# Performance work log

Hardware: AMD Instinct MI355X
Metric: run time of the kernel (lower is better)

Reference implementation:

```python
import jax, jax.numpy as jnp
import numpy as np

B, D = 8192, 128
REGULARIZE = 0.01


def setup_inputs() -> dict:
    key = jax.random.key(0)
    ks = jax.random.split(key, 8)
    s = 1.0 / np.sqrt(D)
    X = jax.random.normal(ks[0], (B, D), dtype=jnp.float32)
    y = jax.random.randint(ks[1], (B,), 0, 100, dtype=jnp.int64 if jax.config.read('jax_enable_x64') else jnp.int32)
    W1 = jax.random.normal(ks[2], (D, D), dtype=jnp.float32) * s
    b1 = jnp.zeros((D,), dtype=jnp.float32)
    W2 = jax.random.normal(ks[3], (D, D), dtype=jnp.float32) * s
    b2 = jnp.zeros((D,), dtype=jnp.float32)
    W3 = jax.random.normal(ks[4], (D, D), dtype=jnp.float32) * s
    b3 = jnp.zeros((D,), dtype=jnp.float32)
    return {"X": X, "W1": W1, "b1": b1, "W2": W2, "b2": b2, "W3": W3, "b3": b3, "y": y}


def _mapper(X, W1, b1, W2, b2, W3, b3):
    h = jax.nn.relu(X @ W1 + b1)
    h = jax.nn.relu(h @ W2 + b2)
    return h @ W3 + b3  # no activation on last layer


def reference(X, W1, b1, W2, b2, W3, b3, y):
    h = _mapper(X, W1, b1, W2, b2, W3, b3)          # (B, D)
    avg_dist = jnp.mean(h ** 2)
    # squared euclidean all-pairs via GEMM trick: ||a-b||^2 = |a|^2 + |b|^2 - 2 a.b
    sq = jnp.sum(h ** 2, axis=-1)                   # (B,)
    dist = jnp.maximum(sq[:, None] + sq[None, :] - 2.0 * (h @ h.T), 0.0)  # (B, B)
    neq = (y[None, :] != y[:, None]).astype(h.dtype)
    eq = 1.0 - neq
    # -mean(neq * log(1.01 - exp(-d))) - mean(eq * log(exp(-d))) ; log(exp(-d)) = -d
    loss = -jnp.mean(neq * jnp.log(1.01 - jnp.exp(-dist))) + jnp.mean(eq * dist)
    loss = loss + REGULARIZE * avg_dist
    return loss
```

## Files before the change

### kernel.cpp

```cpp
#include <hip/hip_runtime.h>
#include <stdint.h>

#define D 128
#define B_ROWS 8192
#define NT 64
#define NPAIRBLK (NT * (NT + 1) / 2)
#define LW 136

typedef __bf16 bf16x8 __attribute__((ext_vector_type(8)));
typedef float f32x4 __attribute__((ext_vector_type(4)));

__global__ __launch_bounds__(512, 2) void mlp_kernel(
    const float* __restrict__ X,
    const float* __restrict__ W1, const float* __restrict__ b1,
    const float* __restrict__ W2, const float* __restrict__ b2,
    const float* __restrict__ W3, const float* __restrict__ b3,
    unsigned short* __restrict__ hb, float* __restrict__ sq)
{
    __shared__ unsigned short actA[32 * LW];
    __shared__ unsigned short actB[32 * LW];

    const int t = threadIdx.x;
    const int lane = t & 63;
    const int w = t >> 6;
    const int row0 = blockIdx.x * 32;
    const int ll = lane & 15;
    const int q  = lane >> 4;
    const int nb0 = w * 16;

    {
        const int r  = t >> 4;
        const int c8 = (t & 15) * 8;
        const float* xp = X + (size_t)(row0 + r) * D + c8;
        float4 v0 = *(const float4*)(xp);
        float4 v1 = *(const float4*)(xp + 4);
        bf16x8 u;
        u[0] = (__bf16)v0.x; u[1] = (__bf16)v0.y; u[2] = (__bf16)v0.z; u[3] = (__bf16)v0.w;
        u[4] = (__bf16)v1.x; u[5] = (__bf16)v1.y; u[6] = (__bf16)v1.z; u[7] = (__bf16)v1.w;
        *(bf16x8*)(actA + r * LW + c8) = u;
    }
    __syncthreads();

    auto layer = [&](const unsigned short* __restrict__ actIn,
                     unsigned short* __restrict__ actOut,
                     const float* __restrict__ Wg,
                     const float* __restrict__ bg, bool do_relu) {
        f32x4 acc0 = {0.f, 0.f, 0.f, 0.f};
        f32x4 acc1 = {0.f, 0.f, 0.f, 0.f};
        #pragma unroll
        for (int kk = 0; kk < 4; ++kk) {
            bf16x8 a0 = *(const bf16x8*)(actIn + ll * LW + kk * 32 + q * 8);
            bf16x8 a1 = *(const bf16x8*)(actIn + (16 + ll) * LW + kk * 32 + q * 8);
            float wv[8];
            #pragma unroll
            for (int j = 0; j < 8; ++j) {
                const int kg = kk * 32 + q * 8 + j;
                wv[j] = Wg[kg * D + nb0 + ll];
            }
            bf16x8 bfrag;
            #pragma unroll
            for (int j = 0; j < 8; ++j) bfrag[j] = (__bf16)wv[j];
            acc0 = __builtin_amdgcn_mfma_f32_16x16x32_bf16(a0, bfrag, acc0, 0, 0, 0);
            acc1 = __builtin_amdgcn_mfma_f32_16x16x32_bf16(a1, bfrag, acc1, 0, 0, 0);
        }
        const float bb = bg[nb0 + ll];
        #pragma unroll
        for (int rr = 0; rr < 4; ++rr) {
            const int m = q * 4 + rr;
            float v0 = acc0[rr] + bb;
            float v1 = acc1[rr] + bb;
            if (do_relu) { v0 = fmaxf(v0, 0.f); v1 = fmaxf(v1, 0.f); }
            *(__bf16*)(actOut + m * LW + nb0 + ll)        = (__bf16)v0;
            *(__bf16*)(actOut + (16 + m) * LW + nb0 + ll) = (__bf16)v1;
        }
    };

    layer(actA, actB, W1, b1, true);
    __syncthreads();
    layer(actB, actA, W2, b2, true);
    __syncthreads();
    layer(actA, actB, W3, b3, false);
    __syncthreads();

    {
        const int r  = t >> 4;
        const int c8 = (t & 15) * 8;
        bf16x8 hv = *(const bf16x8*)(actB + r * LW + c8);
        *(bf16x8*)(hb + (size_t)(row0 + r) * D + c8) = hv;
        float ps = 0.f;
        #pragma unroll
        for (int j = 0; j < 8; ++j) {
            float f = (float)hv[j];
            ps = fmaf(f, f, ps);
        }
        #pragma unroll
        for (int m = 1; m < 16; m <<= 1) ps += __shfl_xor(ps, m, 64);
        if ((t & 15) == 0) sq[row0 + r] = ps;
    }
}

__global__ __launch_bounds__(512, 4) void pair_kernel(
    const unsigned short* __restrict__ hb, const float* __restrict__ sq,
    const int* __restrict__ y, float* __restrict__ partials)
{
    __shared__ unsigned short ldsA[128 * 128];
    __shared__ unsigned short ldsB[128 * 128];
    __shared__ float sA[128], sB[128];
    __shared__ int yA[128], yB[128];
    __shared__ float red[8];

    const int t = threadIdx.x;
    const int lane = t & 63;
    const int w = t >> 6;

    int b = blockIdx.x, ti = 0;
    while (b >= NT - ti) { b -= NT - ti; ++ti; }
    const int tj = ti + b;
    const int i0 = ti * 128, j0 = tj * 128;

    if (t < 128) { sA[t] = sq[i0 + t]; yA[t] = y[i0 + t]; }
    else if (t < 256) { int u = t - 128; sB[u] = sq[j0 + u]; yB[u] = y[j0 + u]; }

    #pragma unroll
    for (int it = 0; it < 8; ++it) {
        const int fbase = w * 512 + it * 64;
        const int f = fbase + lane;
        const int tile = fbase >> 11;
        const int r = (f >> 4) & 127;
        const int c = f & 15;
        const int gc = c ^ (r & 15);
        const unsigned short* src =
            hb + (size_t)((tile ? j0 : i0) + r) * D + gc * 8;
        unsigned short* dstbase =
            (tile ? ldsB : ldsA) + (size_t)(fbase & 2047) * 8;
        __builtin_amdgcn_global_load_lds(
            (const __attribute__((address_space(1))) void*)src,
            (__attribute__((address_space(3))) void*)dstbase, 16, 0, 0);
    }
    __syncthreads();

    f32x4 acc[4][2];
    const f32x4 z4 = {0.f, 0.f, 0.f, 0.f};
    #pragma unroll
    for (int a = 0; a < 4; ++a)
        #pragma unroll
        for (int c = 0; c < 2; ++c) acc[a][c] = z4;

    const int wr = w >> 2, wc = w & 3;
    const int lh = lane >> 4;
    const int ll = lane & 15;

    #pragma unroll
    for (int kk = 0; kk < 4; ++kk) {
        bf16x8 af[4], bfr[2];
        const int clog = kk * 4 + lh;
        const int phys = clog ^ ll;
        #pragma unroll
        for (int tr = 0; tr < 4; ++tr) {
            const int rowl = wr * 64 + tr * 16 + ll;
            af[tr] = *(const bf16x8*)(ldsA + rowl * 128 + phys * 8);
        }
        #pragma unroll
        for (int tc = 0; tc < 2; ++tc) {
            const int rowl = wc * 32 + tc * 16 + ll;
            bfr[tc] = *(const bf16x8*)(ldsB + rowl * 128 + phys * 8);
        }
        #pragma unroll
        for (int tr = 0; tr < 4; ++tr)
            #pragma unroll
            for (int tc = 0; tc < 2; ++tc)
                acc[tr][tc] = __builtin_amdgcn_mfma_f32_16x16x32_bf16(
                    af[tr], bfr[tc], acc[tr][tc], 0, 0, 0);
    }

    float si[16]; int yi[16];
    #pragma unroll
    for (int tr = 0; tr < 4; ++tr)
        #pragma unroll
        for (int rr = 0; rr < 4; ++rr) {
            const int iloc = wr * 64 + tr * 16 + lh * 4 + rr;
            si[tr * 4 + rr] = sA[iloc];
            yi[tr * 4 + rr] = yA[iloc];
        }
    float sj[2]; int yj[2];
    #pragma unroll
    for (int tc = 0; tc < 2; ++tc) {
        const int jloc = wc * 32 + tc * 16 + ll;
        sj[tc] = sB[jloc]; yj[tc] = yB[jloc];
    }

    float s = 0.f;
    #pragma unroll
    for (int tr = 0; tr < 4; ++tr)
        #pragma unroll
        for (int rr = 0; rr < 4; ++rr) {
            const float sii = si[tr * 4 + rr];
            const int   yii = yi[tr * 4 + rr];
            #pragma unroll
            for (int tc = 0; tc < 2; ++tc) {
                const float dot = acc[tr][tc][rr];
                float d = fmaxf(fmaf(-2.f, dot, sii + sj[tc]), 0.f);
                float e = __builtin_amdgcn_exp2f(d * -1.442695041f);
                float nlg = fmaf(e, fmaf(e, 0.49014802f, 0.99009901f), -0.00995033f);
                s += (yii != yj[tc]) ? nlg : d;
            }
        }

    #pragma unroll
    for (int m = 1; m < 64; m <<= 1) s += __shfl_xor(s, m, 64);
    if (lane == 0) red[w] = s;
    __syncthreads();
    if (t == 0) {
        const float wgt = (ti == tj) ? 1.f : 2.f;
        partials[blockIdx.x] = wgt * (red[0] + red[1] + red[2] + red[3] +
                                      red[4] + red[5] + red[6] + red[7]);
    }
}

__global__ __launch_bounds__(256) void reduce_kernel(
    const float* __restrict__ partials, const float* __restrict__ sq,
    float* __restrict__ out)
{
    __shared__ float r1[4], r3[4];
    const int t = threadIdx.x;
    const int lane = t & 63;
    const int w = t >> 6;
    float a1 = 0.f, a3 = 0.f;
    for (int i = t; i < NPAIRBLK; i += 256) a1 += partials[i];
    for (int i = t; i < B_ROWS; i += 256) a3 += sq[i];
    #pragma unroll
    for (int m = 1; m < 64; m <<= 1) {
        a1 += __shfl_xor(a1, m, 64);
        a3 += __shfl_xor(a3, m, 64);
    }
    if (lane == 0) { r1[w] = a1; r3[w] = a3; }
    __syncthreads();
    if (t == 0) {
        const float A1 = r1[0] + r1[1] + r1[2] + r1[3];
        const float A3 = r3[0] + r3[1] + r3[2] + r3[3];
        const float invB2 = 1.0f / (8192.0f * 8192.0f);
        out[0] = A1 * invB2 + 0.01f * A3 / (8192.0f * 128.0f);
    }
}

extern "C" void kernel_launch(void* const* d_in, const int* in_sizes, int n_in,
                              void* d_out, int out_size, void* d_ws, size_t ws_size,
                              hipStream_t stream) {
    (void)in_sizes; (void)n_in; (void)out_size; (void)ws_size;
    const float* X  = (const float*)d_in[0];
    const float* W1 = (const float*)d_in[1];
    const float* b1 = (const float*)d_in[2];
    const float* W2 = (const float*)d_in[3];
    const float* b2 = (const float*)d_in[4];
    const float* W3 = (const float*)d_in[5];
    const float* b3 = (const float*)d_in[6];
    const int*   y  = (const int*)d_in[7];

    char* ws = (char*)d_ws;
    unsigned short* hb = (unsigned short*)ws;
    float* sq = (float*)(ws + (size_t)B_ROWS * D * 2);
    float* partials = (float*)(ws + (size_t)B_ROWS * D * 2 + (size_t)B_ROWS * 4);

    mlp_kernel<<<B_ROWS / 32, 512, 0, stream>>>(X, W1, b1, W2, b2, W3, b3, hb, sq);
    pair_kernel<<<NPAIRBLK, 512, 0, stream>>>(hb, sq, y, partials);
    reduce_kernel<<<1, 256, 0, stream>>>(partials, sq, (float*)d_out);
}
```

Baseline: 103.0 us.

## Make pair kernel persistent with double-buffered LDS prefetch of next tile

Replaces the one-block-per-tile launch of 2080 blocks with 256 persistent blocks, each looping over its share of the tile pairs. While one tile is computed, the next tile's bf16 rows plus its sq and label vectors are prefetched into a second LDS buffer with async global-to-LDS loads. Explicit vmcnt waits and barriers order the two buffers. This aims to hide global load latency and cut per-block launch and setup cost. In exchange it doubles LDS use per block, which lowers occupancy to about one block per CU and leaves the load balance to a fixed stride.

```diff
diff --git a/kernel.cpp b/kernel.cpp
--- a/kernel.cpp
+++ b/kernel.cpp
@@ -5,6 +5,7 @@
 #define B_ROWS 8192
 #define NT 64
 #define NPAIRBLK (NT * (NT + 1) / 2)
+#define NPBLK 256
 #define LW 136
 
 typedef __bf16 bf16x8 __attribute__((ext_vector_type(8)));
@@ -99,121 +100,157 @@
     }
 }
 
-__global__ __launch_bounds__(512, 4) void pair_kernel(
+__global__ __launch_bounds__(512, 2) void pair_kernel(
     const unsigned short* __restrict__ hb, const float* __restrict__ sq,
     const int* __restrict__ y, float* __restrict__ partials)
 {
-    __shared__ unsigned short ldsA[128 * 128];
-    __shared__ unsigned short ldsB[128 * 128];
-    __shared__ float sA[128], sB[128];
-    __shared__ int yA[128], yB[128];
+    __shared__ __align__(16) unsigned short ldsA[2][128 * 128];
+    __shared__ __align__(16) unsigned short ldsB[2][128 * 128];
+    __shared__ __align__(16) float sS[2][2][128];
+    __shared__ __align__(16) int   sY[2][2][128];
     __shared__ float red[8];
 
     const int t = threadIdx.x;
     const int lane = t & 63;
     const int w = t >> 6;
-
-    int b = blockIdx.x, ti = 0;
-    while (b >= NT - ti) { b -= NT - ti; ++ti; }
-    const int tj = ti + b;
-    const int i0 = ti * 128, j0 = tj * 128;
-
-    if (t < 128) { sA[t] = sq[i0 + t]; yA[t] = y[i0 + t]; }
-    else if (t < 256) { int u = t - 128; sB[u] = sq[j0 + u]; yB[u] = y[j0 + u]; }
-
-    #pragma unroll
-    for (int it = 0; it < 8; ++it) {
-        const int fbase = w * 512 + it * 64;
-        const int f = fbase + lane;
-        const int tile = fbase >> 11;
-        const int r = (f >> 4) & 127;
-        const int c = f & 15;
-        const int gc = c ^ (r & 15);
-        const unsigned short* src =
-            hb + (size_t)((tile ? j0 : i0) + r) * D + gc * 8;
-        unsigned short* dstbase =
-            (tile ? ldsB : ldsA) + (size_t)(fbase & 2047) * 8;
-        __builtin_amdgcn_global_load_lds(
-            (const __attribute__((address_space(1))) void*)src,
-            (__attribute__((address_space(3))) void*)dstbase, 16, 0, 0);
-    }
-    __syncthreads();
-
-    f32x4 acc[4][2];
-    const f32x4 z4 = {0.f, 0.f, 0.f, 0.f};
-    #pragma unroll
-    for (int a = 0; a < 4; ++a)
-        #pragma unroll
-        for (int c = 0; c < 2; ++c) acc[a][c] = z4;
+    const int bid = blockIdx.x;
+    const int n = (2080 + 255 - bid) >> 8;
+
+    auto stage = [&](int p, int pb) {
+        int b = p, ti = 0;
+        while (b >= NT - ti) { b -= NT - ti; ++ti; }
+        const int tj = ti + b;
+        const int i0 = ti * 128, j0 = tj * 128;
+        #pragma unroll
+        for (int it = 0; it < 8; ++it) {
+            const int fbase = w * 512 + it * 64;
+            const int f = fbase + lane;
+            const int tile = fbase >> 11;
+            const int r = (f >> 4) & 127;
+            const int c = f & 15;
+            const int gc = c ^ (r & 15);
+            const unsigned short* src =
+                hb + (size_t)((tile ? j0 : i0) + r) * D + gc * 8;
+            unsigned short* dstbase =
+                (tile ? ldsB[pb] : ldsA[pb]) + (size_t)(fbase & 2047) * 8;
+            __builtin_amdgcn_global_load_lds(
+                (const __attribute__((address_space(1))) void*)src,
+                (__attribute__((address_space(3))) void*)dstbase, 16, 0, 0);
+        }
+        {
+            const int sw = w & 3;
+            const void* src;
+            void* dst;
+            if (sw == 0)      { src = (const void*)(sq + i0 + lane * 4); dst = (void*)&sS[pb][0][0]; }
+            else if (sw == 1) { src = (const void*)(sq + j0 + lane * 4); dst = (void*)&sS[pb][1][0]; }
+            else if (sw == 2) { src = (const void*)(y  + i0 + lane * 4); dst = (void*)&sY[pb][0][0]; }
+            else              { src = (const void*)(y  + j0 + lane * 4); dst = (void*)&sY[pb][1][0]; }
+            if (lane < 32)
+                __builtin_amdgcn_global_load_lds(
+                    (const __attribute__((address_space(1))) void*)src,
+                    (__attribute__((address_space(3))) void*)dst, 16, 0, 0);
+        }
+    };
 
     const int wr = w >> 2, wc = w & 3;
     const int lh = lane >> 4;
     const int ll = lane & 15;
 
-    #pragma unroll
-    for (int kk = 0; kk < 4; ++kk) {
-        bf16x8 af[4], bfr[2];
-        const int clog = kk * 4 + lh;
-        const int phys = clog ^ ll;
-        #pragma unroll
-        for (int tr = 0; tr < 4; ++tr) {
-            const int rowl = wr * 64 + tr * 16 + ll;
-            af[tr] = *(const bf16x8*)(ldsA + rowl * 128 + phys * 8);
-        }
+    stage(bid, 0);
+
+    int p = bid;
+    for (int r = 0; r < n; ++r) {
+        const int pb = r & 1;
+        if (r + 1 < n) {
+            stage(p + NPBLK, pb ^ 1);
+            asm volatile("s_waitcnt vmcnt(9)" ::: "memory");
+        } else {
+            asm volatile("s_waitcnt vmcnt(0)" ::: "memory");
+        }
+        __builtin_amdgcn_sched_barrier(0);
+        __builtin_amdgcn_s_barrier();
+        __builtin_amdgcn_sched_barrier(0);
+
+        int b2 = p, ti = 0;
+        while (b2 >= NT - ti) { b2 -= NT - ti; ++ti; }
+        const int tj = ti + b2;
+
+        f32x4 acc[4][2];
+        const f32x4 z4 = {0.f, 0.f, 0.f, 0.f};
+        #pragma unroll
+        for (int a = 0; a < 4; ++a)
+            #pragma unroll
+            for (int c = 0; c < 2; ++c) acc[a][c] = z4;
+
+        #pragma unroll
+        for (int kk = 0; kk < 4; ++kk) {
+            bf16x8 af[4], bfr[2];
+            const int clog = kk * 4 + lh;
+            const int phys = clog ^ ll;
+            #pragma unroll
+            for (int tr = 0; tr < 4; ++tr) {
+                const int rowl = wr * 64 + tr * 16 + ll;
+                af[tr] = *(const bf16x8*)(ldsA[pb] + rowl * 128 + phys * 8);
+            }
+            #pragma unroll
+            for (int tc = 0; tc < 2; ++tc) {
+                const int rowl = wc * 32 + tc * 16 + ll;
+                bfr[tc] = *(const bf16x8*)(ldsB[pb] + rowl * 128 + phys * 8);
+            }
+            #pragma unroll
+            for (int tr = 0; tr < 4; ++tr)
+                #pragma unroll
+                for (int tc = 0; tc < 2; ++tc)
+                    acc[tr][tc] = __builtin_amdgcn_mfma_f32_16x16x32_bf16(
+                        af[tr], bfr[tc], acc[tr][tc], 0, 0, 0);
+        }
+
+        float si[16]; int yi[16];
+        #pragma unroll
+        for (int tr = 0; tr < 4; ++tr)
+            #pragma unroll
+            for (int rr = 0; rr < 4; ++rr) {
+                const int iloc = wr * 64 + tr * 16 + lh * 4 + rr;
+                si[tr * 4 + rr] = sS[pb][0][iloc];
+                yi[tr * 4 + rr] = sY[pb][0][iloc];
+            }
+        float sj[2]; int yj[2];
         #pragma unroll
         for (int tc = 0; tc < 2; ++tc) {
-            const int rowl = wc * 32 + tc * 16 + ll;
-            bfr[tc] = *(const bf16x8*)(ldsB + rowl * 128 + phys * 8);
-        }
+            const int jloc = wc * 32 + tc * 16 + ll;
+            sj[tc] = sS[pb][1][jloc]; yj[tc] = sY[pb][1][jloc];
+        }
+
+        float s = 0.f;
         #pragma unroll
         for (int tr = 0; tr < 4; ++tr)
             #pragma unroll
-            for (int tc = 0; tc < 2; ++tc)
-                acc[tr][tc] = __builtin_amdgcn_mfma_f32_16x16x32_bf16(
-                    af[tr], bfr[tc], acc[tr][tc], 0, 0, 0);
-    }
-
-    float si[16]; int yi[16];
-    #pragma unroll
-    for (int tr = 0; tr < 4; ++tr)
-        #pragma unroll
-        for (int rr = 0; rr < 4; ++rr) {
-            const int iloc = wr * 64 + tr * 16 + lh * 4 + rr;
-            si[tr * 4 + rr] = sA[iloc];
-            yi[tr * 4 + rr] = yA[iloc];
-        }
-    float sj[2]; int yj[2];
-    #pragma unroll
-    for (int tc = 0; tc < 2; ++tc) {
-        const int jloc = wc * 32 + tc * 16 + ll;
-        sj[tc] = sB[jloc]; yj[tc] = yB[jloc];
-    }
-
-    float s = 0.f;
-    #pragma unroll
-    for (int tr = 0; tr < 4; ++tr)
-        #pragma unroll
-        for (int rr = 0; rr < 4; ++rr) {
-            const float sii = si[tr * 4 + rr];
-            const int   yii = yi[tr * 4 + rr];
-            #pragma unroll
-            for (int tc = 0; tc < 2; ++tc) {
-                const float dot = acc[tr][tc][rr];
-                float d = fmaxf(fmaf(-2.f, dot, sii + sj[tc]), 0.f);
-                float e = __builtin_amdgcn_exp2f(d * -1.442695041f);
-                float nlg = fmaf(e, fmaf(e, 0.49014802f, 0.99009901f), -0.00995033f);
-                s += (yii != yj[tc]) ? nlg : d;
-            }
-        }
-
-    #pragma unroll
-    for (int m = 1; m < 64; m <<= 1) s += __shfl_xor(s, m, 64);
-    if (lane == 0) red[w] = s;
-    __syncthreads();
-    if (t == 0) {
-        const float wgt = (ti == tj) ? 1.f : 2.f;
-        partials[blockIdx.x] = wgt * (red[0] + red[1] + red[2] + red[3] +
-                                      red[4] + red[5] + red[6] + red[7]);
+            for (int rr = 0; rr < 4; ++rr) {
+                const float sii = si[tr * 4 + rr];
+                const int   yii = yi[tr * 4 + rr];
+                #pragma unroll
+                for (int tc = 0; tc < 2; ++tc) {
+                    const float dot = acc[tr][tc][rr];
+                    float d = fmaxf(fmaf(-2.f, dot, sii + sj[tc]), 0.f);
+                    float e = __builtin_amdgcn_exp2f(d * -1.442695041f);
+                    float nlg = fmaf(e, fmaf(e, 0.49014802f, 0.99009901f), -0.00995033f);
+                    s += (yii != yj[tc]) ? nlg : d;
+                }
+            }
+
+        #pragma unroll
+        for (int m = 1; m < 64; m <<= 1) s += __shfl_xor(s, m, 64);
+        if (lane == 0) red[w] = s;
+        asm volatile("s_waitcnt lgkmcnt(0)" ::: "memory");
+        __builtin_amdgcn_sched_barrier(0);
+        __builtin_amdgcn_s_barrier();
+        __builtin_amdgcn_sched_barrier(0);
+        if (t == 0) {
+            const float wgt = (ti == tj) ? 1.f : 2.f;
+            partials[p] = wgt * (red[0] + red[1] + red[2] + red[3] +
+                                 red[4] + red[5] + red[6] + red[7]);
+        }
+        p += NPBLK;
     }
 }
 
@@ -262,6 +299,6 @@
     float* partials = (float*)(ws + (size_t)B_ROWS * D * 2 + (size_t)B_ROWS * 4);
 
     mlp_kernel<<<B_ROWS / 32, 512, 0, stream>>>(X, W1, b1, W2, b2, W3, b3, hb, sq);
-    pair_kernel<<<NPAIRBLK, 512, 0, stream>>>(hb, sq, y, partials);
+    pair_kernel<<<NPBLK, 512, 0, stream>>>(hb, sq, y, partials);
     reduce_kernel<<<1, 256, 0, stream>>>(partials, sq, (float*)d_out);
 }
```

Result: slower. 115.0 us (+11.7%).
